# Optimization experiments

Measured on AMD Instinct MI355X. Metric: run time of the kernel, lower is better.

The kernel has to match this reference:

```python
import jax, jax.numpy as jnp
import numpy as np

FEAT = 39
HID = 1024
SEQ = 254
NCLS = 10
FC1 = 100


def setup_inputs() -> dict:
    key = jax.random.key(0)
    ks = jax.random.split(key, 10)
    B = 128
    x = jax.random.normal(ks[0], (B, SEQ, FEAT), dtype=jnp.float32)
    h0 = jax.random.uniform(ks[1], (B, HID), dtype=jnp.float32)
    s_ih = 1.0 / np.sqrt(HID)
    W_ih = jax.random.uniform(ks[2], (HID, FEAT), jnp.float32, -s_ih, s_ih)
    W_hh = jax.random.uniform(ks[3], (HID, HID), jnp.float32, -s_ih, s_ih)
    b_ih = jax.random.uniform(ks[4], (HID,), jnp.float32, -s_ih, s_ih)
    b_hh = jax.random.uniform(ks[5], (HID,), jnp.float32, -s_ih, s_ih)
    s1 = 1.0 / np.sqrt(SEQ * HID)
    W1 = jax.random.uniform(ks[6], (FC1, SEQ * HID), jnp.float32, -s1, s1)
    b1 = jax.random.uniform(ks[7], (FC1,), jnp.float32, -s1, s1)
    s2 = 1.0 / np.sqrt(FC1)
    W2 = jax.random.uniform(ks[8], (NCLS, FC1), jnp.float32, -s2, s2)
    b2 = jax.random.uniform(ks[9], (NCLS,), jnp.float32, -s2, s2)
    return {"x": x, "h0": h0, "W_ih": W_ih, "W_hh": W_hh, "b_ih": b_ih,
            "b_hh": b_hh, "W1": W1, "b1": b1, "W2": W2, "b2": b2}


def reference(x, h0, W_ih, W_hh, b_ih, b_hh, W1, b1, W2, b2):
    B = x.shape[0]
    # time-major: [SEQ, B, FEAT]
    xt = jnp.transpose(x, (1, 0, 2))
    # precompute input projection for all timesteps: [SEQ, B, HID]
    xproj = jnp.einsum('sbf,hf->sbh', xt, W_ih) + b_ih + b_hh

    def step(h, xp):
        h = jnp.tanh(xp + h @ W_hh.T)
        return h, h

    _, outs = jax.lax.scan(step, h0, xproj)  # outs: [SEQ, B, HID]
    feats = jnp.transpose(outs, (1, 0, 2)).reshape(B, SEQ * HID)
    h1 = jax.nn.relu(feats @ W1.T + b1)
    logits = h1 @ W2.T + b2
    return jax.nn.log_softmax(logits, axis=-1)
```

## Files before the change

kernel.cpp:

```cpp
#include <hip/hip_runtime.h>
#include <hip/hip_bf16.h>
#include <stdint.h>
#include <stddef.h>


typedef unsigned short u16;
typedef __attribute__((ext_vector_type(4))) float f32x4;
typedef __attribute__((ext_vector_type(4))) unsigned short u16x4;
typedef __attribute__((ext_vector_type(8))) short short8;

#define SEQ   254
#define BATCH 128
#define HID   1024
#define FEAT  39
#define FC1N  100
#define FC1P  112
#define NCLS  10
#define NBLK_SCAN 128

#define OFF_FLAGS ((size_t)0)
#define OFF_HS    ((size_t)(32 * 1024))
#define OFF_WHH   (OFF_HS + (size_t)(SEQ + 1) * BATCH * HID * 2)
#define OFF_XP    (OFF_WHH + (size_t)HID * HID * 2)
#define OFF_PART  (OFF_XP + (size_t)SEQ * BATCH * HID * 2)

__device__ inline u16 f2bf(float f){
  union { float f; unsigned u; } v; v.f = f;
  unsigned u = v.u;
  u += 0x7fffu + ((u >> 16) & 1u);
  return (u16)(u >> 16);
}
__device__ inline float bf2f(u16 h){
  union { unsigned u; float f; } v; v.u = ((unsigned)h) << 16;
  return v.f;
}
__device__ inline float fast_tanh(float x){
  float e = __expf(2.0f * x);
  return 1.0f - 2.0f / (e + 1.0f);
}

__device__ inline short8 ld_cohx4(const u16* p){
  short8 r;
  asm volatile("global_load_dwordx4 %0, %1, off sc0 sc1" : "=v"(r) : "v"(p) : "memory");
  return r;
}
__device__ inline void st_coh_u16(u16* p, unsigned v){
  asm volatile("global_store_short %0, %1, off sc0 sc1" :: "v"(p), "v"(v) : "memory");
}
__device__ inline void st_coh_i32(int* p, int v){
  asm volatile("global_store_dword %0, %1, off sc0 sc1" :: "v"(p), "v"(v) : "memory");
}
__device__ inline int ld_coh_i32(const int* p){
  int r;
  asm volatile("global_load_dword %0, %1, off sc0 sc1\n\ts_waitcnt vmcnt(0)"
               : "=v"(r) : "v"(p) : "memory");
  return r;
}

__global__ void cvt_f32_bf16_kernel(const float* __restrict__ in, u16* __restrict__ out, int n4){
  int i = blockIdx.x * blockDim.x + threadIdx.x;
  if (i < n4){
    f32x4 v = *(const f32x4*)(in + (size_t)i * 4);
    u16x4 o;
    o[0] = f2bf(v[0]); o[1] = f2bf(v[1]); o[2] = f2bf(v[2]); o[3] = f2bf(v[3]);
    *(u16x4*)(out + (size_t)i * 4) = o;
  }
}

__global__ __launch_bounds__(1024) void xproj_kernel(const float* __restrict__ x,
                                                     const float* __restrict__ W_ih,
                                                     const float* __restrict__ b_ih,
                                                     const float* __restrict__ b_hh,
                                                     u16* __restrict__ xp){
  const int s = blockIdx.x;
  __shared__ float xs[BATCH * (FEAT + 1)];
  for (int i = threadIdx.x; i < BATCH * FEAT; i += 1024){
    int b = i / FEAT, f = i - b * FEAT;
    xs[b * (FEAT + 1) + f] = x[((size_t)b * SEQ + s) * FEAT + f];
  }
  __syncthreads();
  const int h = threadIdx.x;
  float w[FEAT];
  #pragma unroll
  for (int f = 0; f < FEAT; ++f) w[f] = W_ih[h * FEAT + f];
  const float bias = b_ih[h] + b_hh[h];
  for (int b = 0; b < BATCH; ++b){
    float acc = bias;
    #pragma unroll
    for (int f = 0; f < FEAT; ++f) acc += xs[b * (FEAT + 1) + f] * w[f];
    xp[((size_t)s * BATCH + b) * HID + h] = f2bf(acc);
  }
}

__global__ __launch_bounds__(256, 1) void scan_kernel(const u16* __restrict__ whh,
                                                      const u16* __restrict__ xp,
                                                      u16* __restrict__ hs,
                                                      int* __restrict__ flags){
  const int bid  = blockIdx.x;
  const int bgrp = bid & 7;
  const int hgrp = bid >> 3;
  const int wid  = threadIdx.x >> 6;
  const int lane = threadIdx.x & 63;
  const int lr = lane & 15;
  const int lg = lane >> 4;
  const int b_base = bgrp * 16;
  const int h_base = hgrp * 64 + wid * 16;

  short8 breg[32];
  {
    const u16* wp = whh + (size_t)(h_base + lr) * HID + lg * 8;
    #pragma unroll
    for (int kk = 0; kk < 32; ++kk) breg[kk] = *(const short8*)(wp + kk * 32);
  }

  const int arow  = (b_base + lr) * HID + lg * 8;
  const int b_out = b_base + lg * 4;
  const int h_out = h_base + lr;

  int* flag_self = flags + (hgrp * 8 + bgrp) * 64;
  const int* flag_peer = (threadIdx.x < 16) ? (flags + (threadIdx.x * 8 + bgrp) * 64) : flags;

  for (int s = 0; s < SEQ; ++s){
    const u16* hcur = hs + (size_t)s * (BATCH * HID);

    short8 a[32];
    const u16* pa = hcur + arow;
    #pragma unroll
    for (int kk = 0; kk < 32; ++kk) a[kk] = ld_cohx4(pa + kk * 32);

    const u16* xpp = xp + ((size_t)s * BATCH + b_out) * HID + h_out;
    f32x4 acc;
    acc[0] = bf2f(xpp[0]);
    acc[1] = bf2f(xpp[HID]);
    acc[2] = bf2f(xpp[2 * HID]);
    acc[3] = bf2f(xpp[3 * HID]);

    asm volatile("s_waitcnt vmcnt(0)" ::: "memory");
    __builtin_amdgcn_sched_barrier(0);

    #pragma unroll
    for (int kk = 0; kk < 32; ++kk)
      acc = __builtin_amdgcn_mfma_f32_16x16x32_bf16(a[kk], breg[kk], acc, 0, 0, 0);

    u16* hp = hs + (size_t)(s + 1) * (BATCH * HID) + (size_t)b_out * HID + h_out;
    #pragma unroll
    for (int r = 0; r < 4; ++r)
      st_coh_u16(hp + r * HID, (unsigned)f2bf(fast_tanh(acc[r])));

    asm volatile("s_waitcnt vmcnt(0)" ::: "memory");
    __syncthreads();
    if (threadIdx.x == 0) st_coh_i32(flag_self, s + 1);
    if (threadIdx.x < 16){
      while (ld_coh_i32(flag_peer) <= s) __builtin_amdgcn_s_sleep(2);
    }
    __syncthreads();
  }
}

__global__ __launch_bounds__(256) void fc1_kernel(const u16* __restrict__ outs,
                                                  const float* __restrict__ W1,
                                                  float* __restrict__ part){
  const int s = blockIdx.x;
  const int wid  = threadIdx.x >> 6;
  const int lane = threadIdx.x & 63;
  const int lr = lane & 15;
  const int lg = lane >> 4;

  f32x4 acc[2][7];
  const f32x4 zero = {0.f, 0.f, 0.f, 0.f};
  #pragma unroll
  for (int i = 0; i < 2; ++i)
    #pragma unroll
    for (int n = 0; n < 7; ++n) acc[i][n] = zero;

  const u16* pa0 = outs + ((size_t)s * BATCH + wid * 32 + lr) * HID + lg * 8;
  const u16* pa1 = pa0 + 16 * HID;

  for (int kk = 0; kk < 32; ++kk){
    short8 a0 = *(const short8*)(pa0 + kk * 32);
    short8 a1 = *(const short8*)(pa1 + kk * 32);
    #pragma unroll
    for (int nt = 0; nt < 7; ++nt){
      const int j = nt * 16 + lr;
      short8 bf;
      if (j < FC1N){
        const float* wp = W1 + (size_t)j * (SEQ * HID) + (size_t)s * HID + kk * 32 + lg * 8;
        f32x4 w0 = *(const f32x4*)wp;
        f32x4 w1 = *(const f32x4*)(wp + 4);
        #pragma unroll
        for (int r = 0; r < 4; ++r){ bf[r] = (short)f2bf(w0[r]); bf[r + 4] = (short)f2bf(w1[r]); }
      } else {
        #pragma unroll
        for (int r = 0; r < 8; ++r) bf[r] = 0;
      }
      acc[0][nt] = __builtin_amdgcn_mfma_f32_16x16x32_bf16(a0, bf, acc[0][nt], 0, 0, 0);
      acc[1][nt] = __builtin_amdgcn_mfma_f32_16x16x32_bf16(a1, bf, acc[1][nt], 0, 0, 0);
    }
  }

  #pragma unroll
  for (int i = 0; i < 2; ++i)
    #pragma unroll
    for (int nt = 0; nt < 7; ++nt)
      #pragma unroll
      for (int r = 0; r < 4; ++r){
        const int b = wid * 32 + i * 16 + lg * 4 + r;
        const int j = nt * 16 + lr;
        part[((size_t)s * BATCH + b) * FC1P + j] = acc[i][nt][r];
      }
}

__global__ __launch_bounds__(128) void reduce_kernel(const float* __restrict__ part,
                                                     const float* __restrict__ b1,
                                                     const float* __restrict__ W2,
                                                     const float* __restrict__ b2,
                                                     float* __restrict__ out){
  const int b = blockIdx.x;
  const int j = threadIdx.x;
  __shared__ float h1[FC1N];
  __shared__ float lgt[NCLS];

  if (j < FC1P){
    const float* p = part + (size_t)b * FC1P + j;
    float acc = 0.f;
    #pragma unroll 4
    for (int s = 0; s < SEQ; ++s) acc += p[(size_t)s * BATCH * FC1P];
    if (j < FC1N) h1[j] = fmaxf(acc + b1[j], 0.f);
  }
  __syncthreads();
  if (j < NCLS){
    float v = b2[j];
    for (int q = 0; q < FC1N; ++q) v += h1[q] * W2[j * FC1N + q];
    lgt[j] = v;
  }
  __syncthreads();
  if (j < NCLS){
    float m = lgt[0];
    #pragma unroll
    for (int q = 1; q < NCLS; ++q) m = fmaxf(m, lgt[q]);
    float sum = 0.f;
    #pragma unroll
    for (int q = 0; q < NCLS; ++q) sum += __expf(lgt[q] - m);
    out[b * NCLS + j] = lgt[j] - (m + __logf(sum));
  }
}

extern "C" void kernel_launch(void* const* d_in, const int* in_sizes, int n_in,
                              void* d_out, int out_size, void* d_ws, size_t ws_size,
                              hipStream_t stream){
  (void)in_sizes; (void)n_in; (void)out_size; (void)ws_size;
  const float* x   = (const float*)d_in[0];
  const float* h0  = (const float*)d_in[1];
  const float* Wih = (const float*)d_in[2];
  const float* Whh = (const float*)d_in[3];
  const float* bih = (const float*)d_in[4];
  const float* bhh = (const float*)d_in[5];
  const float* W1  = (const float*)d_in[6];
  const float* b1  = (const float*)d_in[7];
  const float* W2  = (const float*)d_in[8];
  const float* b2  = (const float*)d_in[9];
  float* out = (float*)d_out;

  char* ws = (char*)d_ws;
  int*  flags = (int*)(ws + OFF_FLAGS);
  u16*  hs    = (u16*)(ws + OFF_HS);
  u16*  whh   = (u16*)(ws + OFF_WHH);
  u16*  xp    = (u16*)(ws + OFF_XP);
  float* part = (float*)(ws + OFF_PART);

  hipMemsetAsync(flags, 0, 32 * 1024, stream);
  cvt_f32_bf16_kernel<<<1024, 256, 0, stream>>>(Whh, whh, (HID * HID) / 4);
  cvt_f32_bf16_kernel<<<128, 256, 0, stream>>>(h0, hs, (BATCH * HID) / 4);
  xproj_kernel<<<SEQ, 1024, 0, stream>>>(x, Wih, bih, bhh, xp);
  scan_kernel<<<NBLK_SCAN, 256, 0, stream>>>(whh, xp, hs, flags);
  fc1_kernel<<<SEQ, 256, 0, stream>>>(hs + (size_t)BATCH * HID, W1, part);
  reduce_kernel<<<BATCH, 128, 0, stream>>>(part, b1, W2, b2, out);
}
```

Before: 1.719 ms.

## Replace flag barriers in RNN scan with sentinel-polled hidden-state data

The per-step flag store and peer flag spin-wait in the persistent scan kernel are removed. The hidden-state buffer is instead pre-filled with a 0xAA sentinel pattern, and each wave re-polls only the fragments that still contain the sentinel before running its MFMAs. The MFMA operands are swapped so each lane holds four consecutive hidden units, which lets the output be written as one dwordx2 store instead of four short stores. The scheme assumes the sentinel never appears as a genuine bf16 pair, which holds in practice since 0xAAAA decodes to a tiny negative value. It also adds a large memset of the whole hidden-state history before the kernels run.

Result: slower. 2.830 ms (+64.6%).

```diff
diff --git a/kernel.cpp b/kernel.cpp
--- a/kernel.cpp
+++ b/kernel.cpp
@@ -5,6 +5,8 @@
 
 
 typedef unsigned short u16;
+typedef unsigned int u32;
+typedef __attribute__((ext_vector_type(2))) unsigned int u32x2;
 typedef __attribute__((ext_vector_type(4))) float f32x4;
 typedef __attribute__((ext_vector_type(4))) unsigned short u16x4;
 typedef __attribute__((ext_vector_type(8))) short short8;
@@ -17,9 +19,9 @@
 #define FC1P  112
 #define NCLS  10
 #define NBLK_SCAN 128
-
-#define OFF_FLAGS ((size_t)0)
-#define OFF_HS    ((size_t)(32 * 1024))
+#define SENT  0xAAAAAAAAu
+
+#define OFF_HS    ((size_t)0)
 #define OFF_WHH   (OFF_HS + (size_t)(SEQ + 1) * BATCH * HID * 2)
 #define OFF_XP    (OFF_WHH + (size_t)HID * HID * 2)
 #define OFF_PART  (OFF_XP + (size_t)SEQ * BATCH * HID * 2)
@@ -44,17 +46,18 @@
   asm volatile("global_load_dwordx4 %0, %1, off sc0 sc1" : "=v"(r) : "v"(p) : "memory");
   return r;
 }
-__device__ inline void st_coh_u16(u16* p, unsigned v){
-  asm volatile("global_store_short %0, %1, off sc0 sc1" :: "v"(p), "v"(v) : "memory");
-}
-__device__ inline void st_coh_i32(int* p, int v){
-  asm volatile("global_store_dword %0, %1, off sc0 sc1" :: "v"(p), "v"(v) : "memory");
-}
-__device__ inline int ld_coh_i32(const int* p){
-  int r;
-  asm volatile("global_load_dword %0, %1, off sc0 sc1\n\ts_waitcnt vmcnt(0)"
-               : "=v"(r) : "v"(p) : "memory");
-  return r;
+__device__ inline void st_cohx2(u16* p, u32x2 v){
+  asm volatile("global_store_dwordx2 %0, %1, off sc0 sc1" :: "v"(p), "v"(v) : "memory");
+}
+
+__device__ inline bool frag_bad(short8 v){
+  union { short8 s; u32 w[4]; } u; u.s = v;
+  return (u.w[0] == SENT) | (u.w[1] == SENT) | (u.w[2] == SENT) | (u.w[3] == SENT);
+}
+__device__ inline unsigned wave_or32(unsigned v){
+  #pragma unroll
+  for (int i = 1; i < 64; i <<= 1) v |= __shfl_xor(v, i, 64);
+  return __builtin_amdgcn_readfirstlane(v);
 }
 
 __global__ void cvt_f32_bf16_kernel(const float* __restrict__ in, u16* __restrict__ out, int n4){
@@ -94,8 +97,7 @@
 
 __global__ __launch_bounds__(256, 1) void scan_kernel(const u16* __restrict__ whh,
                                                       const u16* __restrict__ xp,
-                                                      u16* __restrict__ hs,
-                                                      int* __restrict__ flags){
+                                                      u16* __restrict__ hs){
   const int bid  = blockIdx.x;
   const int bgrp = bid & 7;
   const int hgrp = bid >> 3;
@@ -113,47 +115,49 @@
     for (int kk = 0; kk < 32; ++kk) breg[kk] = *(const short8*)(wp + kk * 32);
   }
 
-  const int arow  = (b_base + lr) * HID + lg * 8;
-  const int b_out = b_base + lg * 4;
-  const int h_out = h_base + lr;
-
-  int* flag_self = flags + (hgrp * 8 + bgrp) * 64;
-  const int* flag_peer = (threadIdx.x < 16) ? (flags + (threadIdx.x * 8 + bgrp) * 64) : flags;
+  const int arow = (b_base + lr) * HID + lg * 8;
+  const int b_o  = b_base + lr;
+  const int h_o  = h_base + lg * 4;
 
   for (int s = 0; s < SEQ; ++s){
-    const u16* hcur = hs + (size_t)s * (BATCH * HID);
+    const u16* pa = hs + (size_t)s * (BATCH * HID) + arow;
 
     short8 a[32];
-    const u16* pa = hcur + arow;
     #pragma unroll
     for (int kk = 0; kk < 32; ++kk) a[kk] = ld_cohx4(pa + kk * 32);
-
-    const u16* xpp = xp + ((size_t)s * BATCH + b_out) * HID + h_out;
-    f32x4 acc;
-    acc[0] = bf2f(xpp[0]);
-    acc[1] = bf2f(xpp[HID]);
-    acc[2] = bf2f(xpp[2 * HID]);
-    acc[3] = bf2f(xpp[3 * HID]);
-
     asm volatile("s_waitcnt vmcnt(0)" ::: "memory");
     __builtin_amdgcn_sched_barrier(0);
 
+    unsigned bad = 0;
+    #pragma unroll
+    for (int kk = 0; kk < 32; ++kk) bad |= frag_bad(a[kk]) ? (1u << kk) : 0u;
+    bad = wave_or32(bad);
+    while (bad){
+      #pragma unroll
+      for (int kk = 0; kk < 32; ++kk)
+        if (bad & (1u << kk)) a[kk] = ld_cohx4(pa + kk * 32);
+      asm volatile("s_waitcnt vmcnt(0)" ::: "memory");
+      __builtin_amdgcn_sched_barrier(0);
+      unsigned nb = 0;
+      #pragma unroll
+      for (int kk = 0; kk < 32; ++kk)
+        if (bad & (1u << kk)) nb |= frag_bad(a[kk]) ? (1u << kk) : 0u;
+      bad = wave_or32(nb);
+    }
+    __builtin_amdgcn_sched_barrier(0);
+
+    u16x4 xv = *(const u16x4*)(xp + ((size_t)s * BATCH + b_o) * HID + h_o);
+    f32x4 acc;
+    acc[0] = bf2f(xv[0]); acc[1] = bf2f(xv[1]); acc[2] = bf2f(xv[2]); acc[3] = bf2f(xv[3]);
+
     #pragma unroll
     for (int kk = 0; kk < 32; ++kk)
-      acc = __builtin_amdgcn_mfma_f32_16x16x32_bf16(a[kk], breg[kk], acc, 0, 0, 0);
-
-    u16* hp = hs + (size_t)(s + 1) * (BATCH * HID) + (size_t)b_out * HID + h_out;
-    #pragma unroll
-    for (int r = 0; r < 4; ++r)
-      st_coh_u16(hp + r * HID, (unsigned)f2bf(fast_tanh(acc[r])));
-
-    asm volatile("s_waitcnt vmcnt(0)" ::: "memory");
-    __syncthreads();
-    if (threadIdx.x == 0) st_coh_i32(flag_self, s + 1);
-    if (threadIdx.x < 16){
-      while (ld_coh_i32(flag_peer) <= s) __builtin_amdgcn_s_sleep(2);
-    }
-    __syncthreads();
+      acc = __builtin_amdgcn_mfma_f32_16x16x32_bf16(breg[kk], a[kk], acc, 0, 0, 0);
+
+    u32x2 d;
+    d[0] = (u32)f2bf(fast_tanh(acc[0])) | ((u32)f2bf(fast_tanh(acc[1])) << 16);
+    d[1] = (u32)f2bf(fast_tanh(acc[2])) | ((u32)f2bf(fast_tanh(acc[3])) << 16);
+    st_cohx2(hs + (size_t)(s + 1) * (BATCH * HID) + (size_t)b_o * HID + h_o, d);
   }
 }
 
@@ -262,17 +266,16 @@
   float* out = (float*)d_out;
 
   char* ws = (char*)d_ws;
-  int*  flags = (int*)(ws + OFF_FLAGS);
   u16*  hs    = (u16*)(ws + OFF_HS);
   u16*  whh   = (u16*)(ws + OFF_WHH);
   u16*  xp    = (u16*)(ws + OFF_XP);
   float* part = (float*)(ws + OFF_PART);
 
-  hipMemsetAsync(flags, 0, 32 * 1024, stream);
+  hipMemsetAsync(hs + (size_t)BATCH * HID, 0xAA, (size_t)SEQ * BATCH * HID * 2, stream);
   cvt_f32_bf16_kernel<<<1024, 256, 0, stream>>>(Whh, whh, (HID * HID) / 4);
   cvt_f32_bf16_kernel<<<128, 256, 0, stream>>>(h0, hs, (BATCH * HID) / 4);
   xproj_kernel<<<SEQ, 1024, 0, stream>>>(x, Wih, bih, bhh, xp);
-  scan_kernel<<<NBLK_SCAN, 256, 0, stream>>>(whh, xp, hs, flags);
+  scan_kernel<<<NBLK_SCAN, 256, 0, stream>>>(whh, xp, hs);
   fc1_kernel<<<SEQ, 256, 0, stream>>>(hs + (size_t)BATCH * HID, W1, part);
   reduce_kernel<<<BATCH, 128, 0, stream>>>(part, b1, W2, b2, out);
 }
```
